# Performance work log

Hardware: AMD Instinct MI355X
Metric: run time of the kernel (lower is better)

Reference implementation:

```python
import jax, jax.numpy as jnp
import numpy as np

# Dimensions (match init_kwargs / input_specs)
NF, NLOC, NALL = 1, 1024, 2048
N_DIM, E_DIM, A_DIM = 128, 16, 64
NNEI, A_SEL, AXIS = 120, 20, 4

act = jax.nn.silu


def _lin(key, i, o):
    k1, k2 = jax.random.split(key)
    w = jax.random.normal(k1, (i, o), jnp.float32) / np.float32(np.sqrt(i))
    b = jax.random.normal(k2, (o,), jnp.float32) * 0.01
    return w, b


def setup_inputs() -> dict:
    key = jax.random.key(0)
    ks = jax.random.split(key, 16)
    d = {}
    d["node_ebd_ext"] = jax.random.normal(ks[0], (NF, NALL, N_DIM), jnp.float32)
    d["edge_ebd"] = jax.random.normal(ks[1], (NF, NLOC, NNEI, E_DIM), jnp.float32)
    d["h2"] = jax.random.normal(ks[2], (NF, NLOC, NNEI, 3), jnp.float32)
    d["angle_ebd"] = jax.random.normal(ks[3], (NF, NLOC, A_SEL, A_SEL, A_DIM), jnp.float32)
    d["sw"] = jax.random.uniform(ks[4], (NF, NLOC, NNEI), jnp.float32)
    d["a_sw"] = jax.random.uniform(ks[5], (NF, NLOC, A_SEL), jnp.float32)
    d["nlist"] = jax.random.randint(ks[6], (NF, NLOC, NNEI), 0, NALL)
    d["nlist_mask"] = jnp.ones((NF, NLOC, NNEI), bool)
    d["a_nlist_mask"] = jnp.ones((NF, NLOC, A_SEL), bool)
    edge_info_dim = 2 * N_DIM + E_DIM          # 272
    angle_dim = A_DIM + N_DIM + 2 * E_DIM      # 224 (a_compress_rate == 0)
    d["w_node_self"], d["b_node_self"] = _lin(ks[7], N_DIM, N_DIM)
    d["w_node_sym"], d["b_node_sym"] = _lin(ks[8], (N_DIM + E_DIM) * AXIS, N_DIM)
    d["w_node_edge"], d["b_node_edge"] = _lin(ks[9], edge_info_dim, N_DIM)
    d["w_edge_self"], d["b_edge_self"] = _lin(ks[10], edge_info_dim, E_DIM)
    d["w_ea1"], d["b_ea1"] = _lin(ks[11], angle_dim, E_DIM)
    d["w_ea2"], d["b_ea2"] = _lin(ks[12], E_DIM, E_DIM)
    d["w_angle_self"], d["b_angle_self"] = _lin(ks[13], angle_dim, A_DIM)
    # res_residual update style: one learnable residual scale per update branch,
    # init 'const' with update_residual = 0.1
    d["n_res"] = jnp.full((3, N_DIM), 0.1, jnp.float32)  # self, sym, edge-message
    d["e_res"] = jnp.full((2, E_DIM), 0.1, jnp.float32)  # self, angle-message
    d["a_res"] = jnp.full((1, A_DIM), 0.1, jnp.float32)  # self
    return d


def _forward(node_ebd_ext, edge_ebd, h2, angle_ebd, sw, a_sw,
             w_node_self, b_node_self, w_node_sym, b_node_sym,
             w_node_edge, b_node_edge, w_edge_self, b_edge_self,
             w_ea1, b_ea1, w_ea2, b_ea2, w_angle_self, b_angle_self,
             n_res, e_res, a_res, nlist, nlist_mask, a_nlist_mask):
    nf, nall, n_dim = node_ebd_ext.shape
    _, nloc, nnei, e_dim = edge_ebd.shape
    a_sel = angle_ebd.shape[2]
    node_ebd = node_ebd_ext[:, :nloc]

    # gather neighbor node embeddings: nf x nloc x nnei x n_dim
    nei_node = jax.vmap(lambda tbl, idx: tbl[idx])(node_ebd_ext, nlist)
    nei_node = jnp.where(nlist_mask[..., None], nei_node, 0.0)

    # 1) node self update
    node_self_update = act(node_ebd @ w_node_self + b_node_self)

    # 2) node symmetrization update (grrg over both edge and neighbor-node features)
    wgt = (sw * nlist_mask)[..., None]

    def sym(ebd):
        e = ebd * wgt
        hg = jnp.einsum('flni,flnd->flid', h2, e) / np.float32(nnei)  # f,l,3,d
        grrg = jnp.einsum('flid,flia->flda', hg, hg[..., :AXIS]) / np.float32(3.0)
        return grrg.reshape(nf, nloc, -1)

    node_sym_in = jnp.concatenate([sym(nei_node), sym(edge_ebd)], axis=-1)
    node_sym_update = act(node_sym_in @ w_node_sym + b_node_sym)

    # 3) edge info = [node_i, node_j, edge_ij]
    node_i = jnp.broadcast_to(node_ebd[:, :, None, :], (nf, nloc, nnei, n_dim))
    edge_info = jnp.concatenate([node_i, nei_node, edge_ebd], axis=-1)

    # 3a) node <- edge message (sw-weighted mean over neighbors)
    node_edge_update = act(edge_info @ w_node_edge + b_node_edge) * sw[..., None]
    node_edge_update = node_edge_update.sum(axis=-2) / np.float32(nnei)

    node_new = (node_ebd + n_res[0] * node_self_update
                + n_res[1] * node_sym_update + n_res[2] * node_edge_update)

    # 4) edge self update
    edge_self_update = act(edge_info @ w_edge_self + b_edge_self)

    # 5) angle branch (a_compress_rate == 0)
    edge_for_angle = jnp.where(a_nlist_mask[..., None], edge_ebd[:, :, :a_sel, :], 0.0)
    node_angle = jnp.broadcast_to(node_ebd[:, :, None, None, :], (nf, nloc, a_sel, a_sel, n_dim))
    e_ik = jnp.broadcast_to(edge_for_angle[:, :, :, None, :], (nf, nloc, a_sel, a_sel, e_dim))
    e_ij = jnp.broadcast_to(edge_for_angle[:, :, None, :, :], (nf, nloc, a_sel, a_sel, e_dim))
    angle_info = jnp.concatenate([angle_ebd, node_angle, e_ik, e_ij], axis=-1)

    # edge <- angle message: sw-weighted reduce over one angle axis
    ea = act(angle_info @ w_ea1 + b_ea1)  # nf,nloc,a_sel,a_sel,e_dim
    weighted = a_sw[:, :, :, None, None] * a_sw[:, :, None, :, None] * ea
    reduced = weighted.sum(axis=-2) / np.float32(np.sqrt(a_sel))  # nf,nloc,a_sel,e_dim
    pad = jnp.zeros((nf, nloc, nnei - a_sel, e_dim), edge_ebd.dtype)
    padded = jnp.concatenate([reduced, pad], axis=2)
    full_mask = jnp.concatenate(
        [a_nlist_mask, jnp.zeros((nf, nloc, nnei - a_sel), bool)], axis=-1)
    # smooth_edge_update = False: keep original edge ebd where angle mask is off
    padded = jnp.where(full_mask[..., None], padded, edge_ebd)
    edge_angle_update = act(padded @ w_ea2 + b_ea2)

    edge_new = edge_ebd + e_res[0] * edge_self_update + e_res[1] * edge_angle_update

    # angle self update
    angle_self_update = act(angle_info @ w_angle_self + b_angle_self)
    angle_new = angle_ebd + a_res[0] * angle_self_update

    return node_new, edge_new, angle_new


def reference(node_ebd_ext, edge_ebd, h2, angle_ebd, sw, a_sw, nlist, nlist_mask,
              a_nlist_mask, w_node_self, b_node_self, w_node_sym, b_node_sym,
              w_node_edge, b_node_edge, w_edge_self, b_edge_self, w_ea1, b_ea1,
              w_ea2, b_ea2, w_angle_self, b_angle_self, n_res, e_res, a_res):
    return _forward(node_ebd_ext, edge_ebd, h2, angle_ebd, sw, a_sw,
                    w_node_self, b_node_self, w_node_sym, b_node_sym,
                    w_node_edge, b_node_edge, w_edge_self, b_edge_self,
                    w_ea1, b_ea1, w_ea2, b_ea2, w_angle_self, b_angle_self,
                    n_res, e_res, a_res, nlist, nlist_mask, a_nlist_mask)
```

## Files before the change

### kernel.cpp

```cpp
#include <hip/hip_runtime.h>
#include <math.h>

#define NLOC 1024
#define NALL 2048
#define NDIM 128
#define EDIM 16
#define ADIM 64
#define NNEI 120
#define ASEL 20


__device__ __forceinline__ float silu(float x) {
    return x * __builtin_amdgcn_rcpf(1.f + __expf(-x));
}

__device__ __forceinline__ unsigned short f2bf(float f) {
    unsigned int u = __float_as_uint(f);
    u += 0x7fffu + ((u >> 16) & 1u);
    return (unsigned short)(u >> 16);
}

typedef __attribute__((ext_vector_type(8))) short bf16x8;
typedef __attribute__((ext_vector_type(4))) float f32x4;

__global__ __launch_bounds__(256) void k_prep(
    const float* __restrict__ node_ext,
    const float* __restrict__ w_ne, const float* __restrict__ b_ne,
    const float* __restrict__ w_es, const float* __restrict__ b_es,
    const float* __restrict__ w_ea1, const float* __restrict__ b_ea1,
    const float* __restrict__ w_as, const float* __restrict__ b_as,
    float* __restrict__ proj, float* __restrict__ pre_e,
    float* __restrict__ pre_a, unsigned short* __restrict__ wtb)
{
    const int b = blockIdx.x, t = threadIdx.x;
    if (b == 3072) {
        for (int idx = t; idx < 64 * 80; idx += 256) {
            int k = idx / 80, o = idx - k * 80;
            float v = (o < 16) ? w_ea1[k * 16 + o] : w_as[k * 64 + (o - 16)];
            wtb[o * 64 + k] = f2bf(v);
        }
        return;
    }
    __shared__ float x[128];
    const int row = (b < 2048) ? b : (b - 2048);
    if (t < 128) x[t] = node_ext[row * 128 + t];
    __syncthreads();
    if (b < 2048) {
        if (t < 144) {
            float acc = 0.f;
            if (t < 128) {
                for (int k = 0; k < 128; k++) acc += x[k] * w_ne[(128 + k) * 128 + t];
            } else {
                int o = t - 128;
                for (int k = 0; k < 128; k++) acc += x[k] * w_es[(128 + k) * 16 + o];
            }
            proj[b * 144 + t] = acc;
        }
    } else {
        int i = b - 2048;
        if (t < 144) {
            float acc;
            if (t < 128) {
                acc = b_ne[t];
                for (int k = 0; k < 128; k++) acc += x[k] * w_ne[k * 128 + t];
            } else {
                int o = t - 128;
                acc = b_es[o];
                for (int k = 0; k < 128; k++) acc += x[k] * w_es[k * 16 + o];
            }
            pre_e[i * 144 + t] = acc;
        } else if (t < 224) {
            int o = t - 144;
            float acc;
            if (o < 16) {
                acc = b_ea1[o];
                for (int k = 0; k < 128; k++) acc += x[k] * w_ea1[(64 + k) * 16 + o];
            } else {
                int o2 = o - 16;
                acc = b_as[o2];
                for (int k = 0; k < 128; k++) acc += x[k] * w_as[(64 + k) * 64 + o2];
            }
            pre_a[i * 80 + o] = acc;
        }
    }
}

__global__ __launch_bounds__(256, 4) void k_fused(
    const float* __restrict__ angle, const float* __restrict__ edge,
    const float* __restrict__ asw,
    const float* __restrict__ w_ea1, const float* __restrict__ w_as,
    const unsigned short* __restrict__ wtb, const float* __restrict__ pre_a,
    const float* __restrict__ a_res,
    const float* __restrict__ h2, const float* __restrict__ sw,
    const int* __restrict__ nlist, const float* __restrict__ node_ext,
    const float* __restrict__ w_ne, const float* __restrict__ w_es,
    const float* __restrict__ w_ea2, const float* __restrict__ b_ea2,
    const float* __restrict__ e_res,
    const float* __restrict__ proj, const float* __restrict__ pre_e,
    const float* __restrict__ w_ns, const float* __restrict__ b_ns,
    const float* __restrict__ w_sym, const float* __restrict__ b_sym,
    const float* __restrict__ n_res,
    float* __restrict__ out_angle, float* __restrict__ out_edge,
    float* __restrict__ out_node)
{
    const int i = blockIdx.x, t = threadIdx.x;
    const int lane = t & 63, wv = t >> 6;
    const int m = lane & 15, q = lane >> 4;

    __shared__ float edge_s[120 * 17];
    __shared__ float red_s[320];
    __shared__ float asw_s[ASEL];

    union SM {
        struct {
            float eca[ASEL * 80];
            float ecb[ASEL * 80];
            float ares[ADIM];
        } a;
        struct {
            float esu[120 * 17];
            float pre_e[144];
            float wea2[256], bea2[16], eres[32], swv[120], wes[256];
            float neu_part[2][128], neu[128];
            float node[128], hjc[120 * 4];
            float hgN[3 * 128], hgE[3 * 16], sym[576];
            float hgN_part[2][3][128];
            float hgE_part[8][3][16];
            float s2_part[128];
            int   nl[120];
        } e;
    };
    __shared__ SM u;

    bf16x8 bfrag[5][2];
    #pragma unroll
    for (int nt = 0; nt < 5; nt++)
        #pragma unroll
        for (int ks = 0; ks < 2; ks++)
            bfrag[nt][ks] = *(const bf16x8*)&wtb[(nt * 16 + m) * 64 + ks * 32 + q * 8];

    for (int idx = t; idx < 1920; idx += 256) {
        const int j = idx >> 4, k = idx & 15;
        edge_s[j * 17 + k] = edge[(size_t)i * 1920 + idx];
    }
    if (t < ASEL) asw_s[t] = asw[i * ASEL + t];
    if (t < ADIM) u.a.ares[t] = a_res[t];
    for (int idx = t; idx < 320; idx += 256) red_s[idx] = 0.f;
    __syncthreads();

    int mt = wv;
    float4 c0, c1, c2, c3;
    {
        const float* Arow = angle + ((size_t)i * 400 + mt * 16 + m) * 64 + q * 8;
        c0 = *(const float4*)(Arow + 0);
        c1 = *(const float4*)(Arow + 4);
        c2 = *(const float4*)(Arow + 32);
        c3 = *(const float4*)(Arow + 36);
    }

    for (int idx = t; idx < 2 * ASEL * 80; idx += 256) {
        int half = idx / 1600, rem = idx - half * 1600;
        int aa = rem / 80, o = rem - aa * 80;
        float acc = (half == 0) ? pre_a[i * 80 + o] : 0.f;
        if (o < 16) {
            const float* w = w_ea1 + (192 + half * 16) * 16 + o;
            #pragma unroll
            for (int k = 0; k < 16; k++) acc += edge_s[aa * 17 + k] * w[k * 16];
        } else {
            const float* w = w_as + (192 + half * 16) * 64 + (o - 16);
            #pragma unroll
            for (int k = 0; k < 16; k++) acc += edge_s[aa * 17 + k] * w[k * 64];
        }
        if (half == 0) u.a.eca[rem] = acc; else u.a.ecb[rem] = acc;
    }
    __syncthreads();

    for (; mt < 25; mt += 4) {
        const int nmt = mt + 4;
        float4 n0{}, n1{}, n2{}, n3{};
        if (nmt < 25) {
            const float* Arow = angle + ((size_t)i * 400 + nmt * 16 + m) * 64 + q * 8;
            n0 = *(const float4*)(Arow + 0);
            n1 = *(const float4*)(Arow + 4);
            n2 = *(const float4*)(Arow + 32);
            n3 = *(const float4*)(Arow + 36);
        }

        bf16x8 af0, af1;
        af0[0] = (short)f2bf(c0.x); af0[1] = (short)f2bf(c0.y);
        af0[2] = (short)f2bf(c0.z); af0[3] = (short)f2bf(c0.w);
        af0[4] = (short)f2bf(c1.x); af0[5] = (short)f2bf(c1.y);
        af0[6] = (short)f2bf(c1.z); af0[7] = (short)f2bf(c1.w);
        af1[0] = (short)f2bf(c2.x); af1[1] = (short)f2bf(c2.y);
        af1[2] = (short)f2bf(c2.z); af1[3] = (short)f2bf(c2.w);
        af1[4] = (short)f2bf(c3.x); af1[5] = (short)f2bf(c3.y);
        af1[6] = (short)f2bf(c3.z); af1[7] = (short)f2bf(c3.w);

        const int p0 = mt * 16 + q * 4;
        float rez[4][4];
        #pragma unroll
        for (int r = 0; r < 4; r++) {
            const float* ar = angle + ((size_t)i * 400 + p0 + r) * 64 + m - 16;
            #pragma unroll
            for (int nt = 1; nt < 5; nt++) rez[r][nt - 1] = ar[nt * 16];
        }

        f32x4 acc[5];
        #pragma unroll
        for (int nt = 0; nt < 5; nt++) {
            acc[nt] = (f32x4){0.f, 0.f, 0.f, 0.f};
            acc[nt] = __builtin_amdgcn_mfma_f32_16x16x32_bf16(af0, bfrag[nt][0], acc[nt], 0, 0, 0);
            acc[nt] = __builtin_amdgcn_mfma_f32_16x16x32_bf16(af1, bfrag[nt][1], acc[nt], 0, 0, 0);
        }

        #pragma unroll
        for (int r = 0; r < 4; r++) {
            const int p = p0 + r;
            const int a = p / 20;
            const int bb = p - a * 20;
            {
                const float s = acc[0][r] + u.a.eca[a * 80 + m] + u.a.ecb[bb * 80 + m];
                atomicAdd(&red_s[a * 16 + m], asw_s[bb] * silu(s));
            }
            const size_t base = ((size_t)i * 400 + p) * 64;
            #pragma unroll
            for (int nt = 1; nt < 5; nt++) {
                const int o = nt * 16 + m;
                const float s = acc[nt][r] + u.a.eca[a * 80 + o] + u.a.ecb[bb * 80 + o];
                out_angle[base + o - 16] = rez[r][nt - 1] + u.a.ares[o - 16] * silu(s);
            }
        }

        c0 = n0; c1 = n1; c2 = n2; c3 = n3;
    }
    __syncthreads();

    for (int idx = t; idx < 320; idx += 256) {
        const int aa = idx >> 4;
        red_s[idx] *= asw_s[aa] * 0.22360679774997896f;
    }
    __syncthreads();

    if (t < 144) u.e.pre_e[t] = pre_e[i * 144 + t];
    if (t < 128) u.e.node[t] = node_ext[i * 128 + t];
    if (t < 120) {
        u.e.nl[t] = nlist[i * 120 + t];
        const float s = sw[i * 120 + t];
        u.e.swv[t] = s;
        u.e.hjc[t * 4 + 0] = h2[((size_t)i * 120 + t) * 3 + 0] * s;
        u.e.hjc[t * 4 + 1] = h2[((size_t)i * 120 + t) * 3 + 1] * s;
        u.e.hjc[t * 4 + 2] = h2[((size_t)i * 120 + t) * 3 + 2] * s;
        u.e.hjc[t * 4 + 3] = 0.f;
    }
    if (t < 256) u.e.wea2[t] = w_ea2[t];
    if (t < 16) u.e.bea2[t] = b_ea2[t];
    if (t < 32) u.e.eres[t] = e_res[t];
    for (int idx = t; idx < 256; idx += 256) u.e.wes[idx] = w_es[256 * 16 + idx];
    __syncthreads();

    {
        const int o = t & 127, half = t >> 7;
        const int j0 = half * 60, j1 = j0 + 60;
        float w3c[16];
        #pragma unroll
        for (int k = 0; k < 16; k++) w3c[k] = w_ne[(256 + k) * 128 + o];
        const float pe = u.e.pre_e[o];
        float pjA = proj[(size_t)u.e.nl[j0] * 144 + o];
        float pjB = proj[(size_t)u.e.nl[j0 + 1] * 144 + o];
        float accA = 0.f, accB = 0.f;
        for (int j = j0; j < j1; j += 2) {
            float pnA = 0.f, pnB = 0.f;
            if (j + 2 < j1) {
                pnA = proj[(size_t)u.e.nl[j + 2] * 144 + o];
                pnB = proj[(size_t)u.e.nl[j + 3] * 144 + o];
            }
            const float* erA = &edge_s[j * 17];
            const float* erB = &edge_s[(j + 1) * 17];
            float sA = pe + pjA, sB = pe + pjB;
            #pragma unroll
            for (int k = 0; k < 16; k++) { sA += erA[k] * w3c[k]; sB += erB[k] * w3c[k]; }
            accA += silu(sA) * u.e.swv[j];
            accB += silu(sB) * u.e.swv[j + 1];
            pjA = pnA; pjB = pnB;
        }
        u.e.neu_part[half][o] = accA + accB;
    }

    for (int idx = t; idx < 1920; idx += 256) {
        const int j = idx >> 4, oo = idx & 15;
        const int n = u.e.nl[j];
        float s = u.e.pre_e[128 + oo] + proj[(size_t)n * 144 + 128 + oo];
        #pragma unroll
        for (int k = 0; k < 16; k++) s += edge_s[j * 17 + k] * u.e.wes[k * 16 + oo];
        u.e.esu[j * 17 + oo] = silu(s);
    }
    __syncthreads();

    if (t < 128) u.e.neu[t] = (u.e.neu_part[0][t] + u.e.neu_part[1][t]) * (1.f / 120.f);

    {
        const int d = t & 127, half = t >> 7;
        const int j0 = half * 60, j1 = j0 + 60;
        float a0 = 0.f, a1 = 0.f, a2 = 0.f, b0 = 0.f, b1 = 0.f, b2 = 0.f;
        float vA = node_ext[(size_t)u.e.nl[j0] * 128 + d];
        float vB = node_ext[(size_t)u.e.nl[j0 + 1] * 128 + d];
        for (int j = j0; j < j1; j += 2) {
            float vnA = 0.f, vnB = 0.f;
            if (j + 2 < j1) {
                vnA = node_ext[(size_t)u.e.nl[j + 2] * 128 + d];
                vnB = node_ext[(size_t)u.e.nl[j + 3] * 128 + d];
            }
            const float4 hA = *(const float4*)&u.e.hjc[j * 4];
            const float4 hB = *(const float4*)&u.e.hjc[(j + 1) * 4];
            a0 += hA.x * vA; a1 += hA.y * vA; a2 += hA.z * vA;
            b0 += hB.x * vB; b1 += hB.y * vB; b2 += hB.z * vB;
            vA = vnA; vB = vnB;
        }
        u.e.hgN_part[half][0][d] = a0 + b0;
        u.e.hgN_part[half][1][d] = a1 + b1;
        u.e.hgN_part[half][2][d] = a2 + b2;
    }

    if (t < 128) {
        const int d = t & 15, ch = t >> 4;
        const int j0 = ch * 15;
        float a0 = 0.f, a1 = 0.f, a2 = 0.f;
        for (int j = j0; j < j0 + 15; j++) {
            const float v = edge_s[j * 17 + d];
            const float4 hc = *(const float4*)&u.e.hjc[j * 4];
            a0 += hc.x * v; a1 += hc.y * v; a2 += hc.z * v;
        }
        u.e.hgE_part[ch][0][d] = a0;
        u.e.hgE_part[ch][1][d] = a1;
        u.e.hgE_part[ch][2][d] = a2;
    }

    for (int idx = t; idx < 1920; idx += 256) {
        const int j = idx >> 4, o = idx & 15;
        float s = u.e.bea2[o];
        if (j < 20) {
            #pragma unroll
            for (int k = 0; k < 16; k++) s += red_s[j * 16 + k] * u.e.wea2[k * 16 + o];
        } else {
            const float* er = &edge_s[j * 17];
            #pragma unroll
            for (int k = 0; k < 16; k++) s += er[k] * u.e.wea2[k * 16 + o];
        }
        const float eau = silu(s);
        const float ev = edge_s[j * 17 + o];
        out_edge[((size_t)i * 120 + j) * 16 + o] =
            ev + u.e.eres[o] * u.e.esu[j * 17 + o] + u.e.eres[16 + o] * eau;
    }
    __syncthreads();

    if (t < 128) {
        u.e.hgN[0 * 128 + t] = (u.e.hgN_part[0][0][t] + u.e.hgN_part[1][0][t]) * (1.f / 120.f);
        u.e.hgN[1 * 128 + t] = (u.e.hgN_part[0][1][t] + u.e.hgN_part[1][1][t]) * (1.f / 120.f);
        u.e.hgN[2 * 128 + t] = (u.e.hgN_part[0][2][t] + u.e.hgN_part[1][2][t]) * (1.f / 120.f);
    } else if (t < 176) {
        const int c = (t - 128) >> 4, d = (t - 128) & 15;
        float s = 0.f;
        #pragma unroll
        for (int ch = 0; ch < 8; ch++) s += u.e.hgE_part[ch][c][d];
        u.e.hgE[c * 16 + d] = s * (1.f / 120.f);
    }
    __syncthreads();

    for (int idx = t; idx < 576; idx += 256) {
        if (idx < 512) {
            const int d = idx >> 2, a = idx & 3;
            u.e.sym[idx] = (u.e.hgN[d] * u.e.hgN[a] + u.e.hgN[128 + d] * u.e.hgN[128 + a] +
                            u.e.hgN[256 + d] * u.e.hgN[256 + a]) * (1.f / 3.f);
        } else {
            const int r = idx - 512, d = r >> 2, a = r & 3;
            u.e.sym[idx] = (u.e.hgE[d] * u.e.hgE[a] + u.e.hgE[16 + d] * u.e.hgE[16 + a] +
                            u.e.hgE[32 + d] * u.e.hgE[32 + a]) * (1.f / 3.f);
        }
    }
    __syncthreads();

    float s1 = 0.f, s2 = 0.f;
    {
        const int o = t & 127, half = t >> 7;
        if (half == 0) {
            s1 = b_ns[o];
            for (int k = 0; k < 128; k++) s1 += u.e.node[k] * w_ns[k * 128 + o];
            s2 = b_sym[o];
            for (int k = 0; k < 224; k++) s2 += u.e.sym[k] * w_sym[k * 128 + o];
        } else {
            for (int k = 224; k < 576; k++) s2 += u.e.sym[k] * w_sym[k * 128 + o];
            u.e.s2_part[o] = s2;
        }
    }
    __syncthreads();

    if (t < 128) {
        const float nsu = silu(s1);
        const float nsy = silu(s2 + u.e.s2_part[t]);
        out_node[i * 128 + t] = u.e.node[t] + n_res[t] * nsu + n_res[128 + t] * nsy +
                                n_res[256 + t] * u.e.neu[t];
    }
}

extern "C" void kernel_launch(void* const* d_in, const int* in_sizes, int n_in,
                              void* d_out, int out_size, void* d_ws, size_t ws_size,
                              hipStream_t stream)
{
    const float* node_ext = (const float*)d_in[0];
    const float* edge     = (const float*)d_in[1];
    const float* h2       = (const float*)d_in[2];
    const float* angle    = (const float*)d_in[3];
    const float* sw       = (const float*)d_in[4];
    const float* asw      = (const float*)d_in[5];
    const int*   nlist    = (const int*)d_in[6];
    const float* w_ns  = (const float*)d_in[9];  const float* b_ns  = (const float*)d_in[10];
    const float* w_sym = (const float*)d_in[11]; const float* b_sym = (const float*)d_in[12];
    const float* w_ne  = (const float*)d_in[13]; const float* b_ne  = (const float*)d_in[14];
    const float* w_es  = (const float*)d_in[15]; const float* b_es  = (const float*)d_in[16];
    const float* w_ea1 = (const float*)d_in[17]; const float* b_ea1 = (const float*)d_in[18];
    const float* w_ea2 = (const float*)d_in[19]; const float* b_ea2 = (const float*)d_in[20];
    const float* w_as  = (const float*)d_in[21]; const float* b_as  = (const float*)d_in[22];
    const float* n_res = (const float*)d_in[23];
    const float* e_res = (const float*)d_in[24];
    const float* a_res = (const float*)d_in[25];

    float* out_node  = (float*)d_out;
    float* out_edge  = out_node + (size_t)NLOC * NDIM;
    float* out_angle = out_edge + (size_t)NLOC * NNEI * EDIM;

    float* ws      = (float*)d_ws;
    float* proj    = ws;
    float* pre_e   = proj + 2048 * 144;
    float* pre_a   = pre_e + 1024 * 144;
    unsigned short* wtb = (unsigned short*)(pre_a + 1024 * 80);

    k_prep<<<dim3(3073), dim3(256), 0, stream>>>(node_ext, w_ne, b_ne, w_es, b_es,
                                                 w_ea1, b_ea1, w_as, b_as,
                                                 proj, pre_e, pre_a, wtb);
    k_fused<<<dim3(1024), dim3(256), 0, stream>>>(angle, edge, asw, w_ea1, w_as,
                                                  wtb, pre_a, a_res,
                                                  h2, sw, nlist, node_ext,
                                                  w_ne, w_es, w_ea2, b_ea2, e_res,
                                                  proj, pre_e,
                                                  w_ns, b_ns, w_sym, b_sym, n_res,
                                                  out_angle, out_edge, out_node);
}
```

Baseline: 336.0 us.

## Deepen angle prefetch, stage MFMA weights in LDS, pack bf16 conversion, nontemporal stores

Deepens the software prefetch of angle rows from one to two iterations ahead, which raises memory-level parallelism in the angle MFMA loop. The bf16 B fragments move out of registers into padded LDS and are reloaded per iteration to cut register pressure. The A-fragment conversion now uses the packed v_cvt_pk_bf16_f32 instruction instead of the manual rounding code. Output stores for angle and edge become nontemporal. The trade-offs are more LDS traffic per tile, extra registers for the second prefetch buffer, and possibly different rounding in the hardware conversion.

```diff
diff --git a/kernel.cpp b/kernel.cpp
--- a/kernel.cpp
+++ b/kernel.cpp
@@ -22,6 +22,15 @@
 
 typedef __attribute__((ext_vector_type(8))) short bf16x8;
 typedef __attribute__((ext_vector_type(4))) float f32x4;
+
+__device__ __forceinline__ bf16x8 cvt_pk8(float4 lo, float4 hi) {
+    union { unsigned int u[4]; bf16x8 v; } r;
+    asm("v_cvt_pk_bf16_f32 %0, %1, %2" : "=v"(r.u[0]) : "v"(lo.x), "v"(lo.y));
+    asm("v_cvt_pk_bf16_f32 %0, %1, %2" : "=v"(r.u[1]) : "v"(lo.z), "v"(lo.w));
+    asm("v_cvt_pk_bf16_f32 %0, %1, %2" : "=v"(r.u[2]) : "v"(hi.x), "v"(hi.y));
+    asm("v_cvt_pk_bf16_f32 %0, %1, %2" : "=v"(r.u[3]) : "v"(hi.z), "v"(hi.w));
+    return r.v;
+}
 
 __global__ __launch_bounds__(256) void k_prep(
     const float* __restrict__ node_ext,
@@ -116,6 +125,7 @@
             float eca[ASEL * 80];
             float ecb[ASEL * 80];
             float ares[ADIM];
+            unsigned short wt[80 * 72];
         } a;
         struct {
             float esu[120 * 17];
@@ -132,30 +142,32 @@
     };
     __shared__ SM u;
 
-    bf16x8 bfrag[5][2];
-    #pragma unroll
-    for (int nt = 0; nt < 5; nt++)
-        #pragma unroll
-        for (int ks = 0; ks < 2; ks++)
-            bfrag[nt][ks] = *(const bf16x8*)&wtb[(nt * 16 + m) * 64 + ks * 32 + q * 8];
-
     for (int idx = t; idx < 1920; idx += 256) {
         const int j = idx >> 4, k = idx & 15;
         edge_s[j * 17 + k] = edge[(size_t)i * 1920 + idx];
     }
+    for (int idx = t; idx < 80 * 64; idx += 256) {
+        const int o = idx >> 6, k = idx & 63;
+        u.a.wt[o * 72 + k] = wtb[idx];
+    }
     if (t < ASEL) asw_s[t] = asw[i * ASEL + t];
     if (t < ADIM) u.a.ares[t] = a_res[t];
     for (int idx = t; idx < 320; idx += 256) red_s[idx] = 0.f;
     __syncthreads();
 
     int mt = wv;
-    float4 c0, c1, c2, c3;
+    float4 c0, c1, c2, c3, d0, d1, d2, d3;
     {
-        const float* Arow = angle + ((size_t)i * 400 + mt * 16 + m) * 64 + q * 8;
-        c0 = *(const float4*)(Arow + 0);
-        c1 = *(const float4*)(Arow + 4);
-        c2 = *(const float4*)(Arow + 32);
-        c3 = *(const float4*)(Arow + 36);
+        const float* Ar = angle + ((size_t)i * 400 + mt * 16 + m) * 64 + q * 8;
+        c0 = *(const float4*)(Ar + 0);
+        c1 = *(const float4*)(Ar + 4);
+        c2 = *(const float4*)(Ar + 32);
+        c3 = *(const float4*)(Ar + 36);
+        const float* Br = Ar + 4 * 16 * 64;
+        d0 = *(const float4*)(Br + 0);
+        d1 = *(const float4*)(Br + 4);
+        d2 = *(const float4*)(Br + 32);
+        d3 = *(const float4*)(Br + 36);
     }
 
     for (int idx = t; idx < 2 * ASEL * 80; idx += 256) {
@@ -176,25 +188,14 @@
     __syncthreads();
 
     for (; mt < 25; mt += 4) {
-        const int nmt = mt + 4;
-        float4 n0{}, n1{}, n2{}, n3{};
-        if (nmt < 25) {
-            const float* Arow = angle + ((size_t)i * 400 + nmt * 16 + m) * 64 + q * 8;
-            n0 = *(const float4*)(Arow + 0);
-            n1 = *(const float4*)(Arow + 4);
-            n2 = *(const float4*)(Arow + 32);
-            n3 = *(const float4*)(Arow + 36);
-        }
-
-        bf16x8 af0, af1;
-        af0[0] = (short)f2bf(c0.x); af0[1] = (short)f2bf(c0.y);
-        af0[2] = (short)f2bf(c0.z); af0[3] = (short)f2bf(c0.w);
-        af0[4] = (short)f2bf(c1.x); af0[5] = (short)f2bf(c1.y);
-        af0[6] = (short)f2bf(c1.z); af0[7] = (short)f2bf(c1.w);
-        af1[0] = (short)f2bf(c2.x); af1[1] = (short)f2bf(c2.y);
-        af1[2] = (short)f2bf(c2.z); af1[3] = (short)f2bf(c2.w);
-        af1[4] = (short)f2bf(c3.x); af1[5] = (short)f2bf(c3.y);
-        af1[6] = (short)f2bf(c3.z); af1[7] = (short)f2bf(c3.w);
+        float4 e0{}, e1{}, e2{}, e3{};
+        if (mt + 8 < 25) {
+            const float* Ar = angle + ((size_t)i * 400 + (mt + 8) * 16 + m) * 64 + q * 8;
+            e0 = *(const float4*)(Ar + 0);
+            e1 = *(const float4*)(Ar + 4);
+            e2 = *(const float4*)(Ar + 32);
+            e3 = *(const float4*)(Ar + 36);
+        }
 
         const int p0 = mt * 16 + q * 4;
         float rez[4][4];
@@ -205,12 +206,19 @@
             for (int nt = 1; nt < 5; nt++) rez[r][nt - 1] = ar[nt * 16];
         }
 
+        const bf16x8 af0 = cvt_pk8(c0, c1);
+        const bf16x8 af1 = cvt_pk8(c2, c3);
+
+        int wbase = 0;
+        asm volatile("" : "+v"(wbase));
         f32x4 acc[5];
         #pragma unroll
         for (int nt = 0; nt < 5; nt++) {
+            const bf16x8 b0 = *(const bf16x8*)&u.a.wt[wbase + (nt * 16 + m) * 72 + q * 8];
+            const bf16x8 b1 = *(const bf16x8*)&u.a.wt[wbase + (nt * 16 + m) * 72 + 32 + q * 8];
             acc[nt] = (f32x4){0.f, 0.f, 0.f, 0.f};
-            acc[nt] = __builtin_amdgcn_mfma_f32_16x16x32_bf16(af0, bfrag[nt][0], acc[nt], 0, 0, 0);
-            acc[nt] = __builtin_amdgcn_mfma_f32_16x16x32_bf16(af1, bfrag[nt][1], acc[nt], 0, 0, 0);
+            acc[nt] = __builtin_amdgcn_mfma_f32_16x16x32_bf16(af0, b0, acc[nt], 0, 0, 0);
+            acc[nt] = __builtin_amdgcn_mfma_f32_16x16x32_bf16(af1, b1, acc[nt], 0, 0, 0);
         }
 
         #pragma unroll
@@ -227,11 +235,13 @@
             for (int nt = 1; nt < 5; nt++) {
                 const int o = nt * 16 + m;
                 const float s = acc[nt][r] + u.a.eca[a * 80 + o] + u.a.ecb[bb * 80 + o];
-                out_angle[base + o - 16] = rez[r][nt - 1] + u.a.ares[o - 16] * silu(s);
-            }
-        }
-
-        c0 = n0; c1 = n1; c2 = n2; c3 = n3;
+                __builtin_nontemporal_store(rez[r][nt - 1] + u.a.ares[o - 16] * silu(s),
+                                            &out_angle[base + o - 16]);
+            }
+        }
+
+        c0 = d0; c1 = d1; c2 = d2; c3 = d3;
+        d0 = e0; d1 = e1; d2 = e2; d3 = e3;
     }
     __syncthreads();
 
@@ -348,8 +358,9 @@
         }
         const float eau = silu(s);
         const float ev = edge_s[j * 17 + o];
-        out_edge[((size_t)i * 120 + j) * 16 + o] =
-            ev + u.e.eres[o] * u.e.esu[j * 17 + o] + u.e.eres[16 + o] * eau;
+        __builtin_nontemporal_store(
+            ev + u.e.eres[o] * u.e.esu[j * 17 + o] + u.e.eres[16 + o] * eau,
+            &out_edge[((size_t)i * 120 + j) * 16 + o]);
     }
     __syncthreads();
 
```

Measured after the change: 338.9 us. About the same (+0.9%).

## Replace scalar node projection prep with bf16 MFMA GEMM over packed weights

Applied to the files above, without the earlier changes.

The per-row scalar dot-product prep kernel (3073 blocks, one node row each) is replaced by a weight-packing kernel that transposes and converts all projection weights and biases into a bf16 matrix, followed by an MFMA-based GEMM kernel that computes proj, pre_e and pre_a for 16-row tiles. This targets the redundant weight reads and low arithmetic throughput of the scalar prep. It adds a kernel launch and lowers the precision of node inputs and weights to bf16 for these projections.

```diff
diff --git a/kernel.cpp b/kernel.cpp
--- a/kernel.cpp
+++ b/kernel.cpp
@@ -23,64 +23,89 @@
 typedef __attribute__((ext_vector_type(8))) short bf16x8;
 typedef __attribute__((ext_vector_type(4))) float f32x4;
 
-__global__ __launch_bounds__(256) void k_prep(
-    const float* __restrict__ node_ext,
+__global__ __launch_bounds__(256) void k_wt(
     const float* __restrict__ w_ne, const float* __restrict__ b_ne,
     const float* __restrict__ w_es, const float* __restrict__ b_es,
     const float* __restrict__ w_ea1, const float* __restrict__ b_ea1,
     const float* __restrict__ w_as, const float* __restrict__ b_as,
-    float* __restrict__ proj, float* __restrict__ pre_e,
-    float* __restrict__ pre_a, unsigned short* __restrict__ wtb)
+    unsigned short* __restrict__ wtb, unsigned short* __restrict__ wtb2,
+    float* __restrict__ bias)
 {
-    const int b = blockIdx.x, t = threadIdx.x;
-    if (b == 3072) {
-        for (int idx = t; idx < 64 * 80; idx += 256) {
-            int k = idx / 80, o = idx - k * 80;
-            float v = (o < 16) ? w_ea1[k * 16 + o] : w_as[k * 64 + (o - 16)];
-            wtb[o * 64 + k] = f2bf(v);
-        }
-        return;
-    }
-    __shared__ float x[128];
-    const int row = (b < 2048) ? b : (b - 2048);
-    if (t < 128) x[t] = node_ext[row * 128 + t];
-    __syncthreads();
-    if (b < 2048) {
-        if (t < 144) {
-            float acc = 0.f;
-            if (t < 128) {
-                for (int k = 0; k < 128; k++) acc += x[k] * w_ne[(128 + k) * 128 + t];
-            } else {
-                int o = t - 128;
-                for (int k = 0; k < 128; k++) acc += x[k] * w_es[(128 + k) * 16 + o];
-            }
-            proj[b * 144 + t] = acc;
-        }
-    } else {
-        int i = b - 2048;
-        if (t < 144) {
-            float acc;
-            if (t < 128) {
-                acc = b_ne[t];
-                for (int k = 0; k < 128; k++) acc += x[k] * w_ne[k * 128 + t];
-            } else {
-                int o = t - 128;
-                acc = b_es[o];
-                for (int k = 0; k < 128; k++) acc += x[k] * w_es[k * 16 + o];
-            }
-            pre_e[i * 144 + t] = acc;
-        } else if (t < 224) {
-            int o = t - 144;
-            float acc;
-            if (o < 16) {
-                acc = b_ea1[o];
-                for (int k = 0; k < 128; k++) acc += x[k] * w_ea1[(64 + k) * 16 + o];
-            } else {
-                int o2 = o - 16;
-                acc = b_as[o2];
-                for (int k = 0; k < 128; k++) acc += x[k] * w_as[(64 + k) * 64 + o2];
-            }
-            pre_a[i * 80 + o] = acc;
+    const int idx0 = blockIdx.x * 256 + threadIdx.x;
+    const int stride = gridDim.x * 256;
+    for (int idx = idx0; idx < 80 * 64; idx += stride) {
+        const int o = idx >> 6, k = idx & 63;
+        const float v = (o < 16) ? w_ea1[k * 16 + o] : w_as[k * 64 + (o - 16)];
+        wtb[idx] = f2bf(v);
+    }
+    for (int idx = idx0; idx < 368 * 128; idx += stride) {
+        const int o = idx >> 7, k = idx & 127;
+        float v;
+        if (o < 144) {
+            v = (o < 128) ? w_ne[(128 + k) * 128 + o] : w_es[(128 + k) * 16 + (o - 128)];
+        } else if (o < 288) {
+            const int o2 = o - 144;
+            v = (o2 < 128) ? w_ne[k * 128 + o2] : w_es[k * 16 + (o2 - 128)];
+        } else {
+            const int o3 = o - 288;
+            v = (o3 < 16) ? w_ea1[(64 + k) * 16 + o3] : w_as[(64 + k) * 64 + (o3 - 16)];
+        }
+        wtb2[idx] = f2bf(v);
+    }
+    for (int o = idx0; o < 368; o += stride) {
+        float v = 0.f;
+        if (o >= 144 && o < 272)      v = b_ne[o - 144];
+        else if (o >= 272 && o < 288) v = b_es[o - 272];
+        else if (o >= 288 && o < 304) v = b_ea1[o - 288];
+        else if (o >= 304)            v = b_as[o - 304];
+        bias[o] = v;
+    }
+}
+
+__global__ __launch_bounds__(256) void k_prepg(
+    const float* __restrict__ node_ext, const unsigned short* __restrict__ wtb2,
+    const float* __restrict__ bias,
+    float* __restrict__ proj, float* __restrict__ pre_e, float* __restrict__ pre_a)
+{
+    const int b = blockIdx.x;
+    const int mtile = b >> 1, nhalf = b & 1;
+    const int row0 = mtile * 16;
+    const bool full = (mtile < 64);
+    int ntBeg, ntEnd;
+    if (nhalf == 0) { ntBeg = 0;  ntEnd = full ? 12 : 9; }
+    else            { if (!full) return; ntBeg = 12; ntEnd = 23; }
+
+    const int t = threadIdx.x, lane = t & 63, wv = t >> 6;
+    const int m = lane & 15, q = lane >> 4;
+
+    __shared__ unsigned short a_s[16][136];
+    for (int idx = t; idx < 16 * 128; idx += 256) {
+        const int r = idx >> 7, k = idx & 127;
+        a_s[r][k] = f2bf(node_ext[(size_t)(row0 + r) * 128 + k]);
+    }
+    __syncthreads();
+
+    bf16x8 af[4];
+    #pragma unroll
+    for (int ks = 0; ks < 4; ks++)
+        af[ks] = *(const bf16x8*)&a_s[m][ks * 32 + q * 8];
+
+    for (int nt = ntBeg + wv; nt < ntEnd; nt += 4) {
+        f32x4 acc = (f32x4){0.f, 0.f, 0.f, 0.f};
+        #pragma unroll
+        for (int ks = 0; ks < 4; ks++) {
+            const bf16x8 bf = *(const bf16x8*)&wtb2[(size_t)(nt * 16 + m) * 128 + ks * 32 + q * 8];
+            acc = __builtin_amdgcn_mfma_f32_16x16x32_bf16(af[ks], bf, acc, 0, 0, 0);
+        }
+        const int o = nt * 16 + m;
+        const float bi = bias[o];
+        #pragma unroll
+        for (int r = 0; r < 4; r++) {
+            const int row = row0 + q * 4 + r;
+            const float v = acc[r] + bi;
+            if (o < 144)      proj[(size_t)row * 144 + o] = v;
+            else if (o < 288) pre_e[(size_t)row * 144 + (o - 144)] = v;
+            else              pre_a[(size_t)row * 80 + (o - 288)] = v;
         }
     }
 }
@@ -432,11 +457,15 @@
     float* proj    = ws;
     float* pre_e   = proj + 2048 * 144;
     float* pre_a   = pre_e + 1024 * 144;
-    unsigned short* wtb = (unsigned short*)(pre_a + 1024 * 80);
-
-    k_prep<<<dim3(3073), dim3(256), 0, stream>>>(node_ext, w_ne, b_ne, w_es, b_es,
-                                                 w_ea1, b_ea1, w_as, b_as,
-                                                 proj, pre_e, pre_a, wtb);
+    unsigned short* wtb  = (unsigned short*)(pre_a + 1024 * 80);
+    unsigned short* wtb2 = wtb + 80 * 64;
+    float* bias = (float*)(wtb2 + 368 * 128);
+
+    k_wt<<<dim3(128), dim3(256), 0, stream>>>(w_ne, b_ne, w_es, b_es,
+                                              w_ea1, b_ea1, w_as, b_as,
+                                              wtb, wtb2, bias);
+    k_prepg<<<dim3(256), dim3(256), 0, stream>>>(node_ext, wtb2, bias,
+                                                 proj, pre_e, pre_a);
     k_fused<<<dim3(1024), dim3(256), 0, stream>>>(angle, edge, asw, w_ea1, w_as,
                                                   wtb, pre_a, a_res,
                                                   h2, sw, nlist, node_ext,
```

After: 325.5 us. 1.03x faster.
